# Kernel tuning notes

Measured on AMD Instinct MI355X. Metric: run time of the kernel, lower is better.

The kernel has to match this reference:

```python
import jax, jax.numpy as jnp
import numpy as np

NUM_GRAPHS = 64
NEG_SLOPE = 0.2  # DGL GATConv default negative_slope


def _gat_layer(h, W, a_l, a_r, b, src, dst, n_nodes):
    # DGL GATConv, num_heads=1: feat = h @ W (no bias in fc),
    # e_ij = LeakyReLU(a_l . feat_src + a_r . feat_dst), softmax over incoming
    # edges of each dst node, out_dst = sum alpha * feat_src + bias.
    feat = h @ W                      # [N, D]
    el = feat @ a_l                   # [N]
    er = feat @ a_r                   # [N]
    e = jax.nn.leaky_relu(el[src] + er[dst], NEG_SLOPE)   # [E]
    m = jax.ops.segment_max(e, dst, num_segments=n_nodes)  # per-dst max
    ex = jnp.exp(e - m[dst])
    s = jax.ops.segment_sum(ex, dst, num_segments=n_nodes)
    alpha = ex / s[dst]               # edge softmax
    out = jax.ops.segment_sum(feat[src] * alpha[:, None], dst, num_segments=n_nodes)
    return out + b


def setup_inputs() -> dict:
    key = jax.random.key(0)
    ks = jax.random.split(key, 12)
    N, E, D_IN, D_H, C = 100000, 1600000, 128, 128, 2
    h = jax.random.normal(ks[0], (N, D_IN), dtype=jnp.float32)
    src = jax.random.randint(ks[1], (E,), 0, N)
    dst = jax.random.randint(ks[2], (E,), 0, N)
    graph_id = jnp.sort(jax.random.randint(ks[3], (N,), 0, NUM_GRAPHS))
    sc = 1.0 / np.sqrt(D_IN)
    params = {
        'W1': jax.random.normal(ks[4], (D_IN, D_H), dtype=jnp.float32) * sc,
        'al1': jax.random.normal(ks[5], (D_H,), dtype=jnp.float32) * sc,
        'ar1': jax.random.normal(ks[6], (D_H,), dtype=jnp.float32) * sc,
        'b1': jnp.zeros((D_H,), dtype=jnp.float32),
        'W2': jax.random.normal(ks[7], (D_H, D_H), dtype=jnp.float32) * sc,
        'al2': jax.random.normal(ks[8], (D_H,), dtype=jnp.float32) * sc,
        'ar2': jax.random.normal(ks[9], (D_H,), dtype=jnp.float32) * sc,
        'b2': jnp.zeros((D_H,), dtype=jnp.float32),
        'Wfc': jax.random.normal(ks[10], (D_H, C), dtype=jnp.float32) * sc,
        'bfc': jnp.zeros((C,), dtype=jnp.float32),
    }
    return dict(h=h, src=src, dst=dst, graph_id=graph_id, **params)


def reference(h, src, dst, graph_id, W1, al1, ar1, b1, W2, al2, ar2, b2, Wfc, bfc):
    n_nodes = h.shape[0]
    x = jax.nn.relu(_gat_layer(h, W1, al1, ar1, b1, src, dst, n_nodes))
    x = jax.nn.relu(_gat_layer(x, W2, al2, ar2, b2, src, dst, n_nodes))
    # dgl.mean_nodes over the batched graph
    counts = jax.ops.segment_sum(jnp.ones((n_nodes,), x.dtype), graph_id,
                                 num_segments=NUM_GRAPHS)
    hg = jax.ops.segment_sum(x, graph_id, num_segments=NUM_GRAPHS)
    hg = hg / jnp.clip(counts, 1.0)[:, None]          # [G, D]
    logits = hg @ Wfc + bfc                            # [G, C]
    return jax.nn.log_softmax(logits, axis=-1)
```

## Files before the change

### kernel.cpp

```cpp
#include <hip/hip_runtime.h>
#include <math.h>

#define NUM_GRAPHS 64
#define D 128
#define PCHUNK 16
#define MT 64
#define ETILE 4096

typedef __attribute__((ext_vector_type(8))) short bf16x8;
typedef __attribute__((ext_vector_type(4))) float f32x4;
typedef __attribute__((ext_vector_type(2))) float f32x2;

__device__ __forceinline__ unsigned bf16rne(float x) {
    unsigned u = __float_as_uint(x);
    return (u + 0x7fffu + ((u >> 16) & 1u)) >> 16;
}
__device__ __forceinline__ float bflo(unsigned u) { return __uint_as_float(u << 16); }
__device__ __forceinline__ float bfhi(unsigned u) { return __uint_as_float(u & 0xffff0000u); }

__device__ __forceinline__ unsigned encf(float f) {
    unsigned u = __float_as_uint(f);
    return (u & 0x80000000u) ? ~u : (u | 0x80000000u);
}
__device__ __forceinline__ float decf(unsigned e) {
    unsigned u = (e & 0x80000000u) ? (e & 0x7fffffffu) : ~e;
    return __uint_as_float(u);
}


__global__ __launch_bounds__(256) void k_front(
    const int* __restrict__ dst, int* __restrict__ bhist, int E, int nbT,
    const float* __restrict__ W1, const float* __restrict__ W2,
    unsigned short* __restrict__ Wt1, unsigned short* __restrict__ Wt2,
    const int* __restrict__ gid, int* __restrict__ gs, int* __restrict__ ge, int N) {
    __shared__ int h[1024];
    int b = blockIdx.x;
    int tid = threadIdx.x;
    if (b < nbT) {
        for (int i = tid; i < 1024; i += 256) h[i] = 0;
        __syncthreads();
        int e0 = b * ETILE;
        int e1 = min(e0 + ETILE, E);
        for (int i = e0 + tid; i < e1; i += 256) atomicAdd(&h[dst[i] >> 7], 1);
        __syncthreads();
        for (int i = tid; i < 1024; i += 256)
            if (h[i]) atomicAdd(&bhist[i], h[i]);
    } else if (b < nbT + 16) {
        int bb = b - nbT;
        const float* W = (bb & 8) ? W2 : W1;
        unsigned short* Wt = (bb & 8) ? Wt2 : Wt1;
        int n = (bb & 7) * 16 + (tid >> 4);
        int c = tid & 15;
        unsigned v[8];
        #pragma unroll
        for (int j = 0; j < 8; ++j) v[j] = bf16rne(W[(c * 8 + j) * D + n]);
        uint4 pk;
        pk.x = v[0] | (v[1] << 16);
        pk.y = v[2] | (v[3] << 16);
        pk.z = v[4] | (v[5] << 16);
        pk.w = v[6] | (v[7] << 16);
        ((uint4*)Wt)[n * 16 + c] = pk;
    } else {
        int n = (b - nbT - 16) * 256 + tid;
        if (n >= N) return;
        int g = gid[n];
        if (n == 0 || gid[n - 1] != g) gs[g] = n;
        if (n == N - 1 || gid[n + 1] != g) ge[g] = n;
    }
}

__global__ __launch_bounds__(1024) void k_bucket_scan(const int* __restrict__ bhist,
                                                      int* __restrict__ bbase,
                                                      int* __restrict__ bcur,
                                                      int NB, int E,
                                                      int* __restrict__ row_ptr, int N) {
    __shared__ int sm[1024];
    int t = threadIdx.x;
    int v = (t < NB) ? bhist[t] : 0;
    sm[t] = v;
    __syncthreads();
    for (int off = 1; off < 1024; off <<= 1) {
        int y = (t >= off) ? sm[t - off] : 0;
        __syncthreads();
        sm[t] += y;
        __syncthreads();
    }
    if (t < NB) { bbase[t] = sm[t] - v; bcur[t] = sm[t] - v; }
    if (t == 0) { bbase[NB] = E; row_ptr[N] = E; }
}

__global__ __launch_bounds__(256) void k_partition(const int* __restrict__ src,
                                                   const int* __restrict__ dst,
                                                   int* __restrict__ bcur,
                                                   unsigned* __restrict__ part, int E) {
    __shared__ int h[1024];
    __shared__ int cur[1024];
    int tid = threadIdx.x;
    for (int i = tid; i < 1024; i += 256) h[i] = 0;
    __syncthreads();
    int e0 = blockIdx.x * ETILE;
    int e1 = min(e0 + ETILE, E);
    for (int i = e0 + tid; i < e1; i += 256) atomicAdd(&h[dst[i] >> 7], 1);
    __syncthreads();
    for (int i = tid; i < 1024; i += 256) {
        int c = h[i];
        cur[i] = c ? atomicAdd(&bcur[i], c) : 0;
    }
    __syncthreads();
    for (int i = e0 + tid; i < e1; i += 256) {
        int d = dst[i];
        int b = d >> 7;
        int pos = atomicAdd(&cur[b], 1);
        part[pos] = (unsigned)src[i] | ((unsigned)(d & 127) << 17);
    }
}


__global__ __launch_bounds__(256) void k_gemm_mfma_sort(
    const void* __restrict__ Xv, int x_fp32,
    const unsigned short* __restrict__ Wt16,
    const float* __restrict__ al, const float* __restrict__ ar,
    unsigned short* __restrict__ feat16, float* __restrict__ el,
    float* __restrict__ er, unsigned* __restrict__ glmax_u, int N, int gemmBlocks,
    const unsigned* __restrict__ part, const int* __restrict__ bbase,
    int* __restrict__ row_ptr, int* __restrict__ csr_src) {
    __shared__ uint4 WsU[128 * 16];
    __shared__ uint4 XsU[MT * 16];
    __shared__ float smax[4];
    int bx = blockIdx.x;
    int T = gridDim.x;
    int g0 = (int)((long long)bx * gemmBlocks / T);
    int g1 = (int)((long long)(bx + 1) * gemmBlocks / T);
    int tid = threadIdx.x;

    if (g1 == g0) {
        int b = bx - g0;
        int base = bbase[b];
        int bcnt = bbase[b + 1] - base;
        int* ldeg = (int*)XsU;
        int* lcur = ldeg + 128;
        if (tid < 128) ldeg[tid] = 0;
        __syncthreads();
        for (int i = tid; i < bcnt; i += 256)
            atomicAdd(&ldeg[part[base + i] >> 17], 1);
        __syncthreads();
        int myv = (tid < 128) ? ldeg[tid] : 0;
        for (int off = 1; off < 128; off <<= 1) {
            int y = 0;
            if (tid < 128 && tid >= off) y = ldeg[tid - off];
            __syncthreads();
            if (tid < 128) ldeg[tid] += y;
            __syncthreads();
        }
        if (tid < 128) {
            int excl = ldeg[tid] - myv;
            int node = (b << 7) + tid;
            if (node < N) row_ptr[node] = base + excl;
            lcur[tid] = base + excl;
        }
        __syncthreads();
        for (int i = tid; i < bcnt; i += 256) {
            unsigned v = part[base + i];
            int pos = atomicAdd(&lcur[v >> 17], 1);
            csr_src[pos] = (int)(v & 0x1FFFFu);
        }
        return;
    }

    int row0 = g0 * MT;

    for (int idx = tid; idx < 128 * 16; idx += 256) {
        int n = idx >> 4, c = idx & 15;
        WsU[(n << 4) | (c ^ (n & 15))] = ((const uint4*)Wt16)[idx];
    }
    if (x_fp32) {
        const float4* X4 = (const float4*)Xv;
        for (int idx = tid; idx < MT * 16; idx += 256) {
            int n = idx >> 4, c = idx & 15;
            int row = row0 + n;
            uint4 o = make_uint4(0, 0, 0, 0);
            if (row < N) {
                float4 f0 = X4[(size_t)row * 32 + c * 2];
                float4 f1 = X4[(size_t)row * 32 + c * 2 + 1];
                o.x = bf16rne(f0.x) | (bf16rne(f0.y) << 16);
                o.y = bf16rne(f0.z) | (bf16rne(f0.w) << 16);
                o.z = bf16rne(f1.x) | (bf16rne(f1.y) << 16);
                o.w = bf16rne(f1.z) | (bf16rne(f1.w) << 16);
            }
            XsU[(n << 4) | (c ^ (n & 15))] = o;
        }
    } else {
        const uint4* X16 = (const uint4*)Xv;
        for (int idx = tid; idx < MT * 16; idx += 256) {
            int n = idx >> 4, c = idx & 15;
            int row = row0 + n;
            uint4 o = make_uint4(0, 0, 0, 0);
            if (row < N) o = X16[(size_t)row * 16 + c];
            XsU[(n << 4) | (c ^ (n & 15))] = o;
        }
    }
    __syncthreads();

    int lane = tid & 63, w = tid >> 6;
    int quad = lane >> 4, l16 = lane & 15;
    const bf16x8* WsF = (const bf16x8*)WsU;
    const bf16x8* XsF = (const bf16x8*)XsU;
    f32x4 acc[8];
    #pragma unroll
    for (int i = 0; i < 8; ++i) acc[i] = (f32x4){0.f, 0.f, 0.f, 0.f};

    int arow = w * 16 + l16;
    #pragma unroll
    for (int ks = 0; ks < 4; ++ks) {
        int c = ks * 4 + quad;
        bf16x8 A = XsF[(arow << 4) | (c ^ l16)];
        #pragma unroll
        for (int nt = 0; nt < 8; ++nt) {
            bf16x8 B = WsF[((nt * 16 + l16) << 4) | (c ^ l16)];
            acc[nt] = __builtin_amdgcn_mfma_f32_16x16x32_bf16(A, B, acc[nt], 0, 0, 0);
        }
    }

    float alv[8], arv[8];
    #pragma unroll
    for (int nt = 0; nt < 8; ++nt) { alv[nt] = al[nt * 16 + l16]; arv[nt] = ar[nt * 16 + l16]; }
    float lmax = -1e30f;
    #pragma unroll
    for (int r = 0; r < 4; ++r) {
        float pl = 0.f, pr = 0.f;
        #pragma unroll
        for (int nt = 0; nt < 8; ++nt) { pl += acc[nt][r] * alv[nt]; pr += acc[nt][r] * arv[nt]; }
        #pragma unroll
        for (int o = 1; o < 16; o <<= 1) { pl += __shfl_xor(pl, o); pr += __shfl_xor(pr, o); }
        int row = row0 + w * 16 + quad * 4 + r;
        if (l16 == 0 && row < N) { el[row] = pl; er[row] = pr; }
        lmax = fmaxf(lmax, pl);
    }
    lmax = fmaxf(lmax, __shfl_xor(lmax, 16));
    lmax = fmaxf(lmax, __shfl_xor(lmax, 32));
    if (lane == 0) smax[w] = lmax;

    unsigned short* XsS = (unsigned short*)XsU;
    #pragma unroll
    for (int nt = 0; nt < 8; ++nt)
        #pragma unroll
        for (int r = 0; r < 4; ++r) {
            int lrow = w * 16 + quad * 4 + r;
            int col = nt * 16 + l16;
            int ch = col >> 3;
            int sc = ch ^ (lrow & 15);
            XsS[lrow * 128 + sc * 8 + (col & 7)] = (unsigned short)bf16rne(acc[nt][r]);
        }
    __syncthreads();
    if (tid == 0) {
        float bm = fmaxf(fmaxf(smax[0], smax[1]), fmaxf(smax[2], smax[3]));
        atomicMax(glmax_u, encf(bm));
    }
    for (int idx = tid; idx < MT * 16; idx += 256) {
        int n = idx >> 4, c = idx & 15;
        int row = row0 + n;
        if (row < N) ((uint4*)feat16)[(size_t)row * 16 + c] = XsU[(n << 4) | (c ^ (n & 15))];
    }
}


__global__ __launch_bounds__(256) void k_aggregate(
    const unsigned short* __restrict__ feat16, const float* __restrict__ el,
    const float* __restrict__ er, const int* __restrict__ row_ptr,
    const int* __restrict__ csr_src, const float* __restrict__ bias,
    const unsigned* __restrict__ glmax_u, unsigned short* __restrict__ outv, int N) {
    int wid = (blockIdx.x * blockDim.x + threadIdx.x) >> 6;
    int lane = threadIdx.x & 63;
    if (wid >= N) return;
    int beg = row_ptr[wid], end = row_ptr[wid + 1];
    float erd = er[wid];
    float M = decf(glmax_u[0]) + erd;
    M = fmaxf(M, 0.2f * M);

    int qa = lane >> 4, sub = lane & 15;
    const char* fb = (const char*)feat16 + (sub << 4);
    f32x2 a0 = {0.f, 0.f}, a1 = {0.f, 0.f}, a2 = {0.f, 0.f}, a3 = {0.f, 0.f};
    float s = 0.f;
    int j = beg + qa;
    for (; j + 12 < end; j += 16) {
        int sn0 = csr_src[j], sn1 = csr_src[j + 4];
        int sn2 = csr_src[j + 8], sn3 = csr_src[j + 12];
        float t0 = el[sn0] + erd, t1 = el[sn1] + erd;
        float t2 = el[sn2] + erd, t3 = el[sn3] + erd;
        uint4 q0 = *(const uint4*)(fb + ((unsigned)sn0 << 8));
        uint4 q1 = *(const uint4*)(fb + ((unsigned)sn1 << 8));
        uint4 q2 = *(const uint4*)(fb + ((unsigned)sn2 << 8));
        uint4 q3 = *(const uint4*)(fb + ((unsigned)sn3 << 8));
        t0 = fmaxf(t0, 0.2f * t0); t1 = fmaxf(t1, 0.2f * t1);
        t2 = fmaxf(t2, 0.2f * t2); t3 = fmaxf(t3, 0.2f * t3);
        float w0 = __expf(t0 - M), w1 = __expf(t1 - M);
        float w2 = __expf(t2 - M), w3 = __expf(t3 - M);
        s += (w0 + w1) + (w2 + w3);
        f32x2 f;
        f.x = bflo(q0.x); f.y = bfhi(q0.x); a0 += w0 * f;
        f.x = bflo(q0.y); f.y = bfhi(q0.y); a1 += w0 * f;
        f.x = bflo(q0.z); f.y = bfhi(q0.z); a2 += w0 * f;
        f.x = bflo(q0.w); f.y = bfhi(q0.w); a3 += w0 * f;
        f.x = bflo(q1.x); f.y = bfhi(q1.x); a0 += w1 * f;
        f.x = bflo(q1.y); f.y = bfhi(q1.y); a1 += w1 * f;
        f.x = bflo(q1.z); f.y = bfhi(q1.z); a2 += w1 * f;
        f.x = bflo(q1.w); f.y = bfhi(q1.w); a3 += w1 * f;
        f.x = bflo(q2.x); f.y = bfhi(q2.x); a0 += w2 * f;
        f.x = bflo(q2.y); f.y = bfhi(q2.y); a1 += w2 * f;
        f.x = bflo(q2.z); f.y = bfhi(q2.z); a2 += w2 * f;
        f.x = bflo(q2.w); f.y = bfhi(q2.w); a3 += w2 * f;
        f.x = bflo(q3.x); f.y = bfhi(q3.x); a0 += w3 * f;
        f.x = bflo(q3.y); f.y = bfhi(q3.y); a1 += w3 * f;
        f.x = bflo(q3.z); f.y = bfhi(q3.z); a2 += w3 * f;
        f.x = bflo(q3.w); f.y = bfhi(q3.w); a3 += w3 * f;
    }
    for (; j + 4 < end; j += 8) {
        int sn0 = csr_src[j], sn1 = csr_src[j + 4];
        float t0 = el[sn0] + erd, t1 = el[sn1] + erd;
        uint4 q0 = *(const uint4*)(fb + ((unsigned)sn0 << 8));
        uint4 q1 = *(const uint4*)(fb + ((unsigned)sn1 << 8));
        t0 = fmaxf(t0, 0.2f * t0); t1 = fmaxf(t1, 0.2f * t1);
        float w0 = __expf(t0 - M), w1 = __expf(t1 - M);
        s += w0 + w1;
        f32x2 f;
        f.x = bflo(q0.x); f.y = bfhi(q0.x); a0 += w0 * f;
        f.x = bflo(q0.y); f.y = bfhi(q0.y); a1 += w0 * f;
        f.x = bflo(q0.z); f.y = bfhi(q0.z); a2 += w0 * f;
        f.x = bflo(q0.w); f.y = bfhi(q0.w); a3 += w0 * f;
        f.x = bflo(q1.x); f.y = bfhi(q1.x); a0 += w1 * f;
        f.x = bflo(q1.y); f.y = bfhi(q1.y); a1 += w1 * f;
        f.x = bflo(q1.z); f.y = bfhi(q1.z); a2 += w1 * f;
        f.x = bflo(q1.w); f.y = bfhi(q1.w); a3 += w1 * f;
    }
    if (j < end) {
        int sn = csr_src[j];
        float t = el[sn] + erd;
        uint4 q = *(const uint4*)(fb + ((unsigned)sn << 8));
        t = fmaxf(t, 0.2f * t);
        float w = __expf(t - M);
        s += w;
        f32x2 f;
        f.x = bflo(q.x); f.y = bfhi(q.x); a0 += w * f;
        f.x = bflo(q.y); f.y = bfhi(q.y); a1 += w * f;
        f.x = bflo(q.z); f.y = bfhi(q.z); a2 += w * f;
        f.x = bflo(q.w); f.y = bfhi(q.w); a3 += w * f;
    }
    float vr[8] = {a0.x, a0.y, a1.x, a1.y, a2.x, a2.y, a3.x, a3.y};
    #pragma unroll
    for (int c = 0; c < 8; ++c) {
        vr[c] += __shfl_xor(vr[c], 16);
        vr[c] += __shfl_xor(vr[c], 32);
    }
    s += __shfl_xor(s, 16);
    s += __shfl_xor(s, 32);
    float inv = (end > beg) ? 1.f / s : 0.f;
    if (lane < 16) {
        float4 b0 = ((const float4*)bias)[lane * 2];
        float4 b1 = ((const float4*)bias)[lane * 2 + 1];
        float v[8];
        v[0] = fmaxf(vr[0] * inv + b0.x, 0.f);
        v[1] = fmaxf(vr[1] * inv + b0.y, 0.f);
        v[2] = fmaxf(vr[2] * inv + b0.z, 0.f);
        v[3] = fmaxf(vr[3] * inv + b0.w, 0.f);
        v[4] = fmaxf(vr[4] * inv + b1.x, 0.f);
        v[5] = fmaxf(vr[5] * inv + b1.y, 0.f);
        v[6] = fmaxf(vr[6] * inv + b1.z, 0.f);
        v[7] = fmaxf(vr[7] * inv + b1.w, 0.f);
        uint4 pk;
        pk.x = bf16rne(v[0]) | (bf16rne(v[1]) << 16);
        pk.y = bf16rne(v[2]) | (bf16rne(v[3]) << 16);
        pk.z = bf16rne(v[4]) | (bf16rne(v[5]) << 16);
        pk.w = bf16rne(v[6]) | (bf16rne(v[7]) << 16);
        ((uint4*)outv)[(size_t)wid * 16 + lane] = pk;
    }
}


__global__ __launch_bounds__(256) void k_pool_partial(const unsigned short* __restrict__ x,
                                                      const int* __restrict__ gs,
                                                      const int* __restrict__ ge,
                                                      float* __restrict__ hg) {
    int g = blockIdx.x, c = blockIdx.y;
    int start = gs[g], last = ge[g];
    if (start > last) return;
    int sub = threadIdx.x & 15;
    int r   = threadIdx.x >> 4;
    const uint4* x4 = (const uint4*)x;
    float acc[8] = {};
    for (int n = start + c * 16 + r; n <= last; n += PCHUNK * 16) {
        uint4 q = x4[(size_t)n * 16 + sub];
        acc[0] += bflo(q.x); acc[1] += bfhi(q.x);
        acc[2] += bflo(q.y); acc[3] += bfhi(q.y);
        acc[4] += bflo(q.z); acc[5] += bfhi(q.z);
        acc[6] += bflo(q.w); acc[7] += bfhi(q.w);
    }
    __shared__ float sm[256][8];
    #pragma unroll
    for (int k = 0; k < 8; ++k) sm[threadIdx.x][k] = acc[k];
    __syncthreads();
    for (int off = 8; off >= 1; off >>= 1) {
        if (r < off) {
            #pragma unroll
            for (int k = 0; k < 8; ++k)
                sm[threadIdx.x][k] += sm[threadIdx.x + off * 16][k];
        }
        __syncthreads();
    }
    if (r == 0) {
        #pragma unroll
        for (int k = 0; k < 8; ++k)
            atomicAdd(&hg[g * D + sub * 8 + k], sm[sub][k]);
    }
}

__global__ void k_final(const float* __restrict__ hg, const int* __restrict__ gs,
                        const int* __restrict__ ge, const float* __restrict__ Wfc,
                        const float* __restrict__ bfc, float* __restrict__ out) {
    int g = threadIdx.x;
    if (g >= NUM_GRAPHS) return;
    int start = gs[g], last = ge[g];
    float cnt = (start <= last) ? (float)(last - start + 1) : 1.f;
    float ic = 1.f / cnt;
    float l0 = bfc[0], l1 = bfc[1];
    for (int d = 0; d < D; d++) {
        float v = hg[g * D + d] * ic;
        l0 += v * Wfc[2 * d];
        l1 += v * Wfc[2 * d + 1];
    }
    float mm = fmaxf(l0, l1);
    float lse = mm + logf(expf(l0 - mm) + expf(l1 - mm));
    out[2 * g] = l0 - lse;
    out[2 * g + 1] = l1 - lse;
}


extern "C" void kernel_launch(void* const* d_in, const int* in_sizes, int n_in,
                              void* d_out, int out_size, void* d_ws, size_t ws_size,
                              hipStream_t stream) {
    const float* h   = (const float*)d_in[0];
    const int* src   = (const int*)d_in[1];
    const int* dst   = (const int*)d_in[2];
    const int* gid   = (const int*)d_in[3];
    const float* W1  = (const float*)d_in[4];
    const float* al1 = (const float*)d_in[5];
    const float* ar1 = (const float*)d_in[6];
    const float* b1  = (const float*)d_in[7];
    const float* W2  = (const float*)d_in[8];
    const float* al2 = (const float*)d_in[9];
    const float* ar2 = (const float*)d_in[10];
    const float* b2  = (const float*)d_in[11];
    const float* Wfc = (const float*)d_in[12];
    const float* bfc = (const float*)d_in[13];
    float* out = (float*)d_out;

    int N = in_sizes[0] / D;
    int E = in_sizes[1];
    int NB = (N + 127) >> 7;

    char* p = (char*)d_ws;
    unsigned short* feat16  = (unsigned short*)p; p += (size_t)N * D * 2;
    unsigned short* featAgg = (unsigned short*)p; p += (size_t)N * D * 2;
    float* el    = (float*)p; p += (size_t)N * 4;
    float* er    = (float*)p; p += (size_t)N * 4;
    int* row_ptr = (int*)p;   p += (size_t)(N + 4) * 4;
    int* csr_src = (int*)p;   p += (size_t)E * 4;
    unsigned* part = (unsigned*)p; p += (size_t)E * 4;
    int* bhist   = (int*)p;   p += 1028 * 4;
    unsigned* glmaxu = (unsigned*)p; p += 4 * 4;
    float* hg    = (float*)p; p += NUM_GRAPHS * D * 4;
    size_t zbytes = (char*)p - (char*)bhist;
    int* bbase   = (int*)p;   p += 1028 * 4;
    int* bcur    = (int*)p;   p += 1028 * 4;
    int* gs      = (int*)p;   p += NUM_GRAPHS * 4;
    int* ge      = (int*)p;   p += NUM_GRAPHS * 4;
    unsigned short* Wt1 = (unsigned short*)p; p += D * D * 2;
    unsigned short* Wt2 = (unsigned short*)p; p += D * D * 2;

    int nbN = (N + 255) / 256;
    int nbW = (N * 64 + 255) / 256;
    int nbT = (E + ETILE - 1) / ETILE;
    int gemmB = (N + MT - 1) / MT;

    hipMemsetAsync(bhist, 0, zbytes, stream);
    hipMemsetAsync(gs, 0x7f, NUM_GRAPHS * 4, stream);
    hipMemsetAsync(ge, 0xff, NUM_GRAPHS * 4, stream);

    k_front<<<nbT + 16 + nbN, 256, 0, stream>>>(dst, bhist, E, nbT,
                                                W1, W2, Wt1, Wt2, gid, gs, ge, N);
    k_bucket_scan<<<1, 1024, 0, stream>>>(bhist, bbase, bcur, NB, E, row_ptr, N);
    k_partition<<<nbT, 256, 0, stream>>>(src, dst, bcur, part, E);

    k_gemm_mfma_sort<<<gemmB + NB, 256, 0, stream>>>(
        h, 1, Wt1, al1, ar1, feat16, el, er, glmaxu, N, gemmB,
        part, bbase, row_ptr, csr_src);
    k_aggregate<<<nbW, 256, 0, stream>>>(feat16, el, er, row_ptr, csr_src,
                                         b1, glmaxu, featAgg, N);

    k_gemm_mfma_sort<<<gemmB, 256, 0, stream>>>(
        featAgg, 0, Wt2, al2, ar2, feat16, el, er, glmaxu + 1, N, gemmB,
        part, bbase, row_ptr, csr_src);
    k_aggregate<<<nbW, 256, 0, stream>>>(feat16, el, er, row_ptr, csr_src,
                                         b2, glmaxu + 1, featAgg, N);

    k_pool_partial<<<dim3(NUM_GRAPHS, PCHUNK), 256, 0, stream>>>(featAgg, gs, ge, hg);
    k_final<<<1, 64, 0, stream>>>(hg, gs, ge, Wfc, bfc, out);
}
```

Baseline: 360.2 us.

## Fuse mean-pooling into second aggregation and batch edge weights per wave

The aggregation kernel now computes each block of up to 64 edge weights once per wave, one lane per edge, and stores offset/weight pairs in shared memory for the 16-lane feature gathers. Before, each of the four 16-lane quarter-waves repeated the el load and exp for its own edges. For the second layer the output is no longer written to global memory. Instead, each block of four nodes adds its results straight into the per-graph sums with atomics, which removes the separate pooling kernel and the write and re-read of the activations. This adds a block-wide syncthreads and many float atomics, and the pooled sums are rounded differently from the earlier bf16 round trip.

```diff
diff --git a/kernel.cpp b/kernel.cpp
--- a/kernel.cpp
+++ b/kernel.cpp
@@ -3,7 +3,6 @@
 
 #define NUM_GRAPHS 64
 #define D 128
-#define PCHUNK 16
 #define MT 64
 #define ETILE 4096
 
@@ -264,97 +263,126 @@
 }
 
 
+#define EDGE_FMA(q, wgt) { f32x2 f; \
+    f.x = bflo((q).x); f.y = bfhi((q).x); a0 += (wgt) * f; \
+    f.x = bflo((q).y); f.y = bfhi((q).y); a1 += (wgt) * f; \
+    f.x = bflo((q).z); f.y = bfhi((q).z); a2 += (wgt) * f; \
+    f.x = bflo((q).w); f.y = bfhi((q).w); a3 += (wgt) * f; }
+
 __global__ __launch_bounds__(256) void k_aggregate(
     const unsigned short* __restrict__ feat16, const float* __restrict__ el,
     const float* __restrict__ er, const int* __restrict__ row_ptr,
     const int* __restrict__ csr_src, const float* __restrict__ bias,
-    const unsigned* __restrict__ glmax_u, unsigned short* __restrict__ outv, int N) {
-    int wid = (blockIdx.x * blockDim.x + threadIdx.x) >> 6;
-    int lane = threadIdx.x & 63;
-    if (wid >= N) return;
-    int beg = row_ptr[wid], end = row_ptr[wid + 1];
-    float erd = er[wid];
+    const unsigned* __restrict__ glmax_u, unsigned short* __restrict__ outv,
+    const int* __restrict__ gid, float* __restrict__ hgp, int N) {
+    __shared__ uint2 swo[4][64];
+    __shared__ float bacc[4][16][8];
+    __shared__ int gsm[4];
+    int tid = threadIdx.x;
+    int wv = tid >> 6;
+    int lane = tid & 63;
+    int wid = blockIdx.x * 4 + wv;
+    bool act = wid < N;
+
+    int beg = 0, end = 0;
+    float erd = 0.f;
+    if (act) { beg = row_ptr[wid]; end = row_ptr[wid + 1]; erd = er[wid]; }
     float M = decf(glmax_u[0]) + erd;
     M = fmaxf(M, 0.2f * M);
 
     int qa = lane >> 4, sub = lane & 15;
-    const char* fb = (const char*)feat16 + (sub << 4);
+    unsigned subo = (unsigned)(sub << 4);
+    const char* fb = (const char*)feat16;
     f32x2 a0 = {0.f, 0.f}, a1 = {0.f, 0.f}, a2 = {0.f, 0.f}, a3 = {0.f, 0.f};
     float s = 0.f;
-    int j = beg + qa;
-    for (; j + 12 < end; j += 16) {
-        int sn0 = csr_src[j], sn1 = csr_src[j + 4];
-        int sn2 = csr_src[j + 8], sn3 = csr_src[j + 12];
-        float t0 = el[sn0] + erd, t1 = el[sn1] + erd;
-        float t2 = el[sn2] + erd, t3 = el[sn3] + erd;
-        uint4 q0 = *(const uint4*)(fb + ((unsigned)sn0 << 8));
-        uint4 q1 = *(const uint4*)(fb + ((unsigned)sn1 << 8));
-        uint4 q2 = *(const uint4*)(fb + ((unsigned)sn2 << 8));
-        uint4 q3 = *(const uint4*)(fb + ((unsigned)sn3 << 8));
-        t0 = fmaxf(t0, 0.2f * t0); t1 = fmaxf(t1, 0.2f * t1);
-        t2 = fmaxf(t2, 0.2f * t2); t3 = fmaxf(t3, 0.2f * t3);
-        float w0 = __expf(t0 - M), w1 = __expf(t1 - M);
-        float w2 = __expf(t2 - M), w3 = __expf(t3 - M);
-        s += (w0 + w1) + (w2 + w3);
-        f32x2 f;
-        f.x = bflo(q0.x); f.y = bfhi(q0.x); a0 += w0 * f;
-        f.x = bflo(q0.y); f.y = bfhi(q0.y); a1 += w0 * f;
-        f.x = bflo(q0.z); f.y = bfhi(q0.z); a2 += w0 * f;
-        f.x = bflo(q0.w); f.y = bfhi(q0.w); a3 += w0 * f;
-        f.x = bflo(q1.x); f.y = bfhi(q1.x); a0 += w1 * f;
-        f.x = bflo(q1.y); f.y = bfhi(q1.y); a1 += w1 * f;
-        f.x = bflo(q1.z); f.y = bfhi(q1.z); a2 += w1 * f;
-        f.x = bflo(q1.w); f.y = bfhi(q1.w); a3 += w1 * f;
-        f.x = bflo(q2.x); f.y = bfhi(q2.x); a0 += w2 * f;
-        f.x = bflo(q2.y); f.y = bfhi(q2.y); a1 += w2 * f;
-        f.x = bflo(q2.z); f.y = bfhi(q2.z); a2 += w2 * f;
-        f.x = bflo(q2.w); f.y = bfhi(q2.w); a3 += w2 * f;
-        f.x = bflo(q3.x); f.y = bfhi(q3.x); a0 += w3 * f;
-        f.x = bflo(q3.y); f.y = bfhi(q3.y); a1 += w3 * f;
-        f.x = bflo(q3.z); f.y = bfhi(q3.z); a2 += w3 * f;
-        f.x = bflo(q3.w); f.y = bfhi(q3.w); a3 += w3 * f;
-    }
-    for (; j + 4 < end; j += 8) {
-        int sn0 = csr_src[j], sn1 = csr_src[j + 4];
-        float t0 = el[sn0] + erd, t1 = el[sn1] + erd;
-        uint4 q0 = *(const uint4*)(fb + ((unsigned)sn0 << 8));
-        uint4 q1 = *(const uint4*)(fb + ((unsigned)sn1 << 8));
-        t0 = fmaxf(t0, 0.2f * t0); t1 = fmaxf(t1, 0.2f * t1);
-        float w0 = __expf(t0 - M), w1 = __expf(t1 - M);
-        s += w0 + w1;
-        f32x2 f;
-        f.x = bflo(q0.x); f.y = bfhi(q0.x); a0 += w0 * f;
-        f.x = bflo(q0.y); f.y = bfhi(q0.y); a1 += w0 * f;
-        f.x = bflo(q0.z); f.y = bfhi(q0.z); a2 += w0 * f;
-        f.x = bflo(q0.w); f.y = bfhi(q0.w); a3 += w0 * f;
-        f.x = bflo(q1.x); f.y = bfhi(q1.x); a0 += w1 * f;
-        f.x = bflo(q1.y); f.y = bfhi(q1.y); a1 += w1 * f;
-        f.x = bflo(q1.z); f.y = bfhi(q1.z); a2 += w1 * f;
-        f.x = bflo(q1.w); f.y = bfhi(q1.w); a3 += w1 * f;
-    }
-    if (j < end) {
-        int sn = csr_src[j];
-        float t = el[sn] + erd;
-        uint4 q = *(const uint4*)(fb + ((unsigned)sn << 8));
-        t = fmaxf(t, 0.2f * t);
-        float w = __expf(t - M);
-        s += w;
-        f32x2 f;
-        f.x = bflo(q.x); f.y = bfhi(q.x); a0 += w * f;
-        f.x = bflo(q.y); f.y = bfhi(q.y); a1 += w * f;
-        f.x = bflo(q.z); f.y = bfhi(q.z); a2 += w * f;
-        f.x = bflo(q.w); f.y = bfhi(q.w); a3 += w * f;
-    }
+
+    for (int base = beg; base < end; base += 64) {
+        int nblk = end - base;
+        if (nblk > 64) nblk = 64;
+        unsigned off = 0;
+        float wgt = 0.f;
+        if (lane < nblk) {
+            int sn = csr_src[base + lane];
+            float t = el[sn] + erd;
+            t = fmaxf(t, 0.2f * t);
+            wgt = __expf(t - M);
+            off = ((unsigned)sn) << 8;
+        }
+        s += wgt;
+        swo[wv][lane] = make_uint2(off, __float_as_uint(wgt));
+        int jj = 0;
+        for (; jj + 16 <= nblk; jj += 16) {
+            uint2 r0 = swo[wv][jj + qa];
+            uint2 r1 = swo[wv][jj + 4 + qa];
+            uint2 r2 = swo[wv][jj + 8 + qa];
+            uint2 r3 = swo[wv][jj + 12 + qa];
+            uint4 q0 = *(const uint4*)(fb + (size_t)(r0.x | subo));
+            uint4 q1 = *(const uint4*)(fb + (size_t)(r1.x | subo));
+            uint4 q2 = *(const uint4*)(fb + (size_t)(r2.x | subo));
+            uint4 q3 = *(const uint4*)(fb + (size_t)(r3.x | subo));
+            float w0 = __uint_as_float(r0.y), w1 = __uint_as_float(r1.y);
+            float w2 = __uint_as_float(r2.y), w3 = __uint_as_float(r3.y);
+            EDGE_FMA(q0, w0) EDGE_FMA(q1, w1) EDGE_FMA(q2, w2) EDGE_FMA(q3, w3)
+        }
+        if (jj + 8 <= nblk) {
+            uint2 r0 = swo[wv][jj + qa];
+            uint2 r1 = swo[wv][jj + 4 + qa];
+            uint4 q0 = *(const uint4*)(fb + (size_t)(r0.x | subo));
+            uint4 q1 = *(const uint4*)(fb + (size_t)(r1.x | subo));
+            float w0 = __uint_as_float(r0.y), w1 = __uint_as_float(r1.y);
+            EDGE_FMA(q0, w0) EDGE_FMA(q1, w1)
+            jj += 8;
+        }
+        for (int j2 = jj + qa; j2 < nblk; j2 += 4) {
+            uint2 r = swo[wv][j2];
+            uint4 q = *(const uint4*)(fb + (size_t)(r.x | subo));
+            float w0 = __uint_as_float(r.y);
+            EDGE_FMA(q, w0)
+        }
+    }
+
     float vr[8] = {a0.x, a0.y, a1.x, a1.y, a2.x, a2.y, a3.x, a3.y};
     #pragma unroll
     for (int c = 0; c < 8; ++c) {
         vr[c] += __shfl_xor(vr[c], 16);
         vr[c] += __shfl_xor(vr[c], 32);
     }
-    s += __shfl_xor(s, 16);
-    s += __shfl_xor(s, 32);
+    #pragma unroll
+    for (int o = 1; o < 64; o <<= 1) s += __shfl_xor(s, o);
     float inv = (end > beg) ? 1.f / s : 0.f;
-    if (lane < 16) {
+
+    if (hgp) {
+        if (lane < 16) {
+            float4 b0 = ((const float4*)bias)[lane * 2];
+            float4 b1 = ((const float4*)bias)[lane * 2 + 1];
+            float* bw = bacc[wv][lane];
+            bw[0] = fmaxf(vr[0] * inv + b0.x, 0.f);
+            bw[1] = fmaxf(vr[1] * inv + b0.y, 0.f);
+            bw[2] = fmaxf(vr[2] * inv + b0.z, 0.f);
+            bw[3] = fmaxf(vr[3] * inv + b0.w, 0.f);
+            bw[4] = fmaxf(vr[4] * inv + b1.x, 0.f);
+            bw[5] = fmaxf(vr[5] * inv + b1.y, 0.f);
+            bw[6] = fmaxf(vr[6] * inv + b1.z, 0.f);
+            bw[7] = fmaxf(vr[7] * inv + b1.w, 0.f);
+        }
+        if (lane == 0) gsm[wv] = act ? gid[wid] : -1;
+        __syncthreads();
+        if (tid < 128) {
+            int g0 = gsm[0];
+            bool uni = (gsm[1] == g0) && (gsm[2] == g0) && (gsm[3] == g0) && (g0 >= 0);
+            int sb = tid >> 3, k = tid & 7;
+            if (uni) {
+                float sum = bacc[0][sb][k] + bacc[1][sb][k] + bacc[2][sb][k] + bacc[3][sb][k];
+                atomicAdd(&hgp[g0 * D + tid], sum);
+            } else {
+                #pragma unroll
+                for (int u = 0; u < 4; ++u) {
+                    int g = gsm[u];
+                    if (g >= 0) atomicAdd(&hgp[g * D + tid], bacc[u][sb][k]);
+                }
+            }
+        }
+    } else if (act && lane < 16) {
         float4 b0 = ((const float4*)bias)[lane * 2];
         float4 b1 = ((const float4*)bias)[lane * 2 + 1];
         float v[8];
@@ -375,43 +403,6 @@
     }
 }
 
-
-__global__ __launch_bounds__(256) void k_pool_partial(const unsigned short* __restrict__ x,
-                                                      const int* __restrict__ gs,
-                                                      const int* __restrict__ ge,
-                                                      float* __restrict__ hg) {
-    int g = blockIdx.x, c = blockIdx.y;
-    int start = gs[g], last = ge[g];
-    if (start > last) return;
-    int sub = threadIdx.x & 15;
-    int r   = threadIdx.x >> 4;
-    const uint4* x4 = (const uint4*)x;
-    float acc[8] = {};
-    for (int n = start + c * 16 + r; n <= last; n += PCHUNK * 16) {
-        uint4 q = x4[(size_t)n * 16 + sub];
-        acc[0] += bflo(q.x); acc[1] += bfhi(q.x);
-        acc[2] += bflo(q.y); acc[3] += bfhi(q.y);
-        acc[4] += bflo(q.z); acc[5] += bfhi(q.z);
-        acc[6] += bflo(q.w); acc[7] += bfhi(q.w);
-    }
-    __shared__ float sm[256][8];
-    #pragma unroll
-    for (int k = 0; k < 8; ++k) sm[threadIdx.x][k] = acc[k];
-    __syncthreads();
-    for (int off = 8; off >= 1; off >>= 1) {
-        if (r < off) {
-            #pragma unroll
-            for (int k = 0; k < 8; ++k)
-                sm[threadIdx.x][k] += sm[threadIdx.x + off * 16][k];
-        }
-        __syncthreads();
-    }
-    if (r == 0) {
-        #pragma unroll
-        for (int k = 0; k < 8; ++k)
-            atomicAdd(&hg[g * D + sub * 8 + k], sm[sub][k]);
-    }
-}
 
 __global__ void k_final(const float* __restrict__ hg, const int* __restrict__ gs,
                         const int* __restrict__ ge, const float* __restrict__ Wfc,
@@ -494,14 +485,13 @@
         h, 1, Wt1, al1, ar1, feat16, el, er, glmaxu, N, gemmB,
         part, bbase, row_ptr, csr_src);
     k_aggregate<<<nbW, 256, 0, stream>>>(feat16, el, er, row_ptr, csr_src,
-                                         b1, glmaxu, featAgg, N);
+                                         b1, glmaxu, featAgg, gid, nullptr, N);
 
     k_gemm_mfma_sort<<<gemmB, 256, 0, stream>>>(
         featAgg, 0, Wt2, al2, ar2, feat16, el, er, glmaxu + 1, N, gemmB,
         part, bbase, row_ptr, csr_src);
     k_aggregate<<<nbW, 256, 0, stream>>>(feat16, el, er, row_ptr, csr_src,
-                                         b2, glmaxu + 1, featAgg, N);
-
-    k_pool_partial<<<dim3(NUM_GRAPHS, PCHUNK), 256, 0, stream>>>(featAgg, gs, ge, hg);
+                                         b2, glmaxu + 1, nullptr, gid, hg, N);
+
     k_final<<<1, 64, 0, stream>>>(hg, gs, ge, Wfc, bfc, out);
 }
```

Measured after the change: 392.5 us. +9.0%, slower.

## Fuse mean-pool accumulation into second-layer aggregate kernel

Applied to the files above, without the earlier changes.

The second GAT aggregation no longer writes its bf16 node features. Instead each block reduces its four nodes' ReLU outputs in shared memory and atomically adds them into the per-graph sum buffer, with a fast path when all four nodes belong to the same graph. This removes the separate pooling kernel, its launch, and a full write and read of the node feature matrix. In exchange it adds a block barrier per aggregate block and many float atomics concentrated on a few graph rows, which may contend.

```diff
diff --git a/kernel.cpp b/kernel.cpp
--- a/kernel.cpp
+++ b/kernel.cpp
@@ -3,7 +3,6 @@
 
 #define NUM_GRAPHS 64
 #define D 128
-#define PCHUNK 16
 #define MT 64
 #define ETILE 4096
 
@@ -268,12 +267,19 @@
     const unsigned short* __restrict__ feat16, const float* __restrict__ el,
     const float* __restrict__ er, const int* __restrict__ row_ptr,
     const int* __restrict__ csr_src, const float* __restrict__ bias,
-    const unsigned* __restrict__ glmax_u, unsigned short* __restrict__ outv, int N) {
-    int wid = (blockIdx.x * blockDim.x + threadIdx.x) >> 6;
-    int lane = threadIdx.x & 63;
-    if (wid >= N) return;
-    int beg = row_ptr[wid], end = row_ptr[wid + 1];
-    float erd = er[wid];
+    const unsigned* __restrict__ glmax_u, unsigned short* __restrict__ outv,
+    const int* __restrict__ gid, float* __restrict__ hgp, int N) {
+    __shared__ float bacc[4][16][8];
+    __shared__ int gsm[4];
+    int tid = threadIdx.x;
+    int wv = tid >> 6;
+    int lane = tid & 63;
+    int wid = blockIdx.x * 4 + wv;
+    bool act = wid < N;
+
+    int beg = 0, end = 0;
+    float erd = 0.f;
+    if (act) { beg = row_ptr[wid]; end = row_ptr[wid + 1]; erd = er[wid]; }
     float M = decf(glmax_u[0]) + erd;
     M = fmaxf(M, 0.2f * M);
 
@@ -354,7 +360,39 @@
     s += __shfl_xor(s, 16);
     s += __shfl_xor(s, 32);
     float inv = (end > beg) ? 1.f / s : 0.f;
-    if (lane < 16) {
+
+    if (hgp) {
+        if (lane < 16) {
+            float4 b0 = ((const float4*)bias)[lane * 2];
+            float4 b1 = ((const float4*)bias)[lane * 2 + 1];
+            float* bw = bacc[wv][lane];
+            bw[0] = fmaxf(vr[0] * inv + b0.x, 0.f);
+            bw[1] = fmaxf(vr[1] * inv + b0.y, 0.f);
+            bw[2] = fmaxf(vr[2] * inv + b0.z, 0.f);
+            bw[3] = fmaxf(vr[3] * inv + b0.w, 0.f);
+            bw[4] = fmaxf(vr[4] * inv + b1.x, 0.f);
+            bw[5] = fmaxf(vr[5] * inv + b1.y, 0.f);
+            bw[6] = fmaxf(vr[6] * inv + b1.z, 0.f);
+            bw[7] = fmaxf(vr[7] * inv + b1.w, 0.f);
+        }
+        if (lane == 0) gsm[wv] = act ? gid[wid] : -1;
+        __syncthreads();
+        if (tid < 128) {
+            int g0 = gsm[0];
+            bool uni = (gsm[1] == g0) && (gsm[2] == g0) && (gsm[3] == g0) && (g0 >= 0);
+            int sb = tid >> 3, k = tid & 7;
+            if (uni) {
+                float sum = bacc[0][sb][k] + bacc[1][sb][k] + bacc[2][sb][k] + bacc[3][sb][k];
+                atomicAdd(&hgp[g0 * D + tid], sum);
+            } else {
+                #pragma unroll
+                for (int u = 0; u < 4; ++u) {
+                    int g = gsm[u];
+                    if (g >= 0) atomicAdd(&hgp[g * D + tid], bacc[u][sb][k]);
+                }
+            }
+        }
+    } else if (act && lane < 16) {
         float4 b0 = ((const float4*)bias)[lane * 2];
         float4 b1 = ((const float4*)bias)[lane * 2 + 1];
         float v[8];
@@ -375,43 +413,6 @@
     }
 }
 
-
-__global__ __launch_bounds__(256) void k_pool_partial(const unsigned short* __restrict__ x,
-                                                      const int* __restrict__ gs,
-                                                      const int* __restrict__ ge,
-                                                      float* __restrict__ hg) {
-    int g = blockIdx.x, c = blockIdx.y;
-    int start = gs[g], last = ge[g];
-    if (start > last) return;
-    int sub = threadIdx.x & 15;
-    int r   = threadIdx.x >> 4;
-    const uint4* x4 = (const uint4*)x;
-    float acc[8] = {};
-    for (int n = start + c * 16 + r; n <= last; n += PCHUNK * 16) {
-        uint4 q = x4[(size_t)n * 16 + sub];
-        acc[0] += bflo(q.x); acc[1] += bfhi(q.x);
-        acc[2] += bflo(q.y); acc[3] += bfhi(q.y);
-        acc[4] += bflo(q.z); acc[5] += bfhi(q.z);
-        acc[6] += bflo(q.w); acc[7] += bfhi(q.w);
-    }
-    __shared__ float sm[256][8];
-    #pragma unroll
-    for (int k = 0; k < 8; ++k) sm[threadIdx.x][k] = acc[k];
-    __syncthreads();
-    for (int off = 8; off >= 1; off >>= 1) {
-        if (r < off) {
-            #pragma unroll
-            for (int k = 0; k < 8; ++k)
-                sm[threadIdx.x][k] += sm[threadIdx.x + off * 16][k];
-        }
-        __syncthreads();
-    }
-    if (r == 0) {
-        #pragma unroll
-        for (int k = 0; k < 8; ++k)
-            atomicAdd(&hg[g * D + sub * 8 + k], sm[sub][k]);
-    }
-}
 
 __global__ void k_final(const float* __restrict__ hg, const int* __restrict__ gs,
                         const int* __restrict__ ge, const float* __restrict__ Wfc,
@@ -494,14 +495,13 @@
         h, 1, Wt1, al1, ar1, feat16, el, er, glmaxu, N, gemmB,
         part, bbase, row_ptr, csr_src);
     k_aggregate<<<nbW, 256, 0, stream>>>(feat16, el, er, row_ptr, csr_src,
-                                         b1, glmaxu, featAgg, N);
+                                         b1, glmaxu, featAgg, gid, nullptr, N);
 
     k_gemm_mfma_sort<<<gemmB, 256, 0, stream>>>(
         featAgg, 0, Wt2, al2, ar2, feat16, el, er, glmaxu + 1, N, gemmB,
         part, bbase, row_ptr, csr_src);
     k_aggregate<<<nbW, 256, 0, stream>>>(feat16, el, er, row_ptr, csr_src,
-                                         b2, glmaxu + 1, featAgg, N);
-
-    k_pool_partial<<<dim3(NUM_GRAPHS, PCHUNK), 256, 0, stream>>>(featAgg, gs, ge, hg);
+                                         b2, glmaxu + 1, nullptr, gid, hg, N);
+
     k_final<<<1, 64, 0, stream>>>(hg, gs, ge, Wfc, bfc, out);
 }
```

After: 395.6 us. +9.8%, slower.
